# Performance work log

Hardware: AMD Instinct MI355X
Metric: run time of the kernel (lower is better)

Reference implementation:

```python
import jax, jax.numpy as jnp
import numpy as np

NUM_HEADS = 4

def _pos_encoding(seq_len, d, dtype):
    # standard sinusoidal positional encoding [seq_len, d]
    pos = jnp.arange(seq_len, dtype=jnp.float32)[:, None]
    i = jnp.arange(0, d, 2, dtype=jnp.float32)
    div = jnp.exp(-jnp.log(10000.0) * i / d)
    ang = pos * div
    pe = jnp.zeros((seq_len, d), jnp.float32)
    pe = pe.at[:, 0::2].set(jnp.sin(ang)).at[:, 1::2].set(jnp.cos(ang))
    return pe.astype(dtype)

def _layer_norm(x, g, b, eps=1e-5):
    m = jnp.mean(x, axis=-1, keepdims=True)
    v = jnp.mean(jnp.square(x - m), axis=-1, keepdims=True)
    return (x - m) / jnp.sqrt(v + eps) * g + b

def setup_inputs() -> dict:
    key = jax.random.key(0)
    ks = jax.random.split(key, 10)
    B, S, H, W, N = 8, 512, 768, 8, 4096
    s = 0.02
    token_reps = jax.random.normal(ks[0], (B, S, H), jnp.float32)
    starts = jax.random.randint(ks[1], (B, N), 0, S - W)
    widths = jax.random.randint(ks[2], (B, N), 1, W + 1)
    span_ids = jnp.stack([starts, starts + widths], axis=-1)  # end > start, end <= S
    span_masks = jax.random.randint(ks[3], (B, N), 0, 2)
    return dict(
        token_reps=token_reps,
        dummy_query=jax.random.normal(ks[4], (H,), jnp.float32) * s,
        in_proj_w=jax.random.normal(ks[5], (3 * H, H), jnp.float32) * s,
        in_proj_b=jnp.zeros((3 * H,), jnp.float32),
        out_w=jax.random.normal(ks[6], (H, H), jnp.float32) * s,
        out_b=jnp.zeros((H,), jnp.float32),
        ln_g=jnp.ones((H,), jnp.float32),
        ln_b=jnp.zeros((H,), jnp.float32),
        ffn_w1=jax.random.normal(ks[7], (H, 4 * H), jnp.float32) * s,
        ffn_b1=jnp.zeros((4 * H,), jnp.float32),
        ffn_w2=jax.random.normal(ks[8], (4 * H, H), jnp.float32) * s,
        ffn_b2=jnp.zeros((H,), jnp.float32),
        span_ids=span_ids,
        span_masks=span_masks,
    )

def reference(token_reps, dummy_query, in_proj_w, in_proj_b, out_w, out_b,
              ln_g, ln_b, ffn_w1, ffn_b1, ffn_w2, ffn_b2, span_ids, span_masks):
    B, S, H = token_reps.shape
    N = span_ids.shape[1]
    NH = NUM_HEADS
    DH = H // NH
    # sequence positional encoding (dropout is identity in eval mode)
    x = token_reps + _pos_encoding(S, H, token_reps.dtype)[None]
    Wq, Wk, Wv = jnp.split(in_proj_w, 3, axis=0)
    bq, bk, bv = jnp.split(in_proj_b, 3)
    # single shared dummy query -> per-head query [NH, DH]
    q = (dummy_query @ Wq.T + bq).reshape(NH, DH)
    k = (x @ Wk.T + bk).reshape(B, S, NH, DH)
    v = (x @ Wv.T + bv).reshape(B, S, NH, DH)
    # scores are identical across spans since the query is shared: [B, NH, S]
    scores = jnp.einsum('hd,bshd->bhs', q, k) / jnp.sqrt(jnp.asarray(DH, x.dtype))
    pos = jnp.arange(S)
    # per-span key validity: start <= pos < end, and span not masked out  [B, N, S]
    valid = (pos[None, None, :] >= span_ids[..., 0:1]) & \
            (pos[None, None, :] < span_ids[..., 1:2]) & \
            (span_masks[..., None] != 0)
    logits = jnp.where(valid[:, :, None, :], scores[:, None, :, :], -1e9)  # [B,N,NH,S]
    w = jax.nn.softmax(logits, axis=-1)
    attn = jnp.einsum('bnhs,bshd->bnhd', w, v).reshape(B, N, H)
    attn = attn @ out_w.T + out_b
    h1 = _layer_norm(attn + dummy_query, ln_g, ln_b)
    ffn = jax.nn.relu(h1 @ ffn_w1 + ffn_b1) @ ffn_w2 + ffn_b2
    out = _layer_norm(ffn + h1, ln_g, ln_b)
    # masked spans produce exact zeros, matching the original loop
    return out * (span_masks[..., None] != 0).astype(out.dtype)
```

## Files before the change

### kernel.cpp

```cpp
#include <hip/hip_runtime.h>
#include <hip/hip_bf16.h>

#define Bb 8
#define Ss 512
#define Hh 768
#define NHh 4
#define Nn 4096
#define ROWS (Bb * Nn)
#define SCB 128

typedef _Float16 f16x8 __attribute__((ext_vector_type(8)));
typedef _Float16 f16x4 __attribute__((ext_vector_type(4)));
typedef _Float16 f16x2 __attribute__((ext_vector_type(2)));
typedef float f32x4 __attribute__((ext_vector_type(4)));

#define DEVINL __device__ __forceinline__

DEVINL void gld_lds16(const void* g, void* l) {
  __builtin_amdgcn_global_load_lds(
      (const __attribute__((address_space(1))) void*)g,
      (__attribute__((address_space(3))) void*)l, 16, 0, 0);
}

template <int V>
DEVINL void wait_vmcnt() {
  if constexpr (V == 0) asm volatile("s_waitcnt vmcnt(0)" ::: "memory");
  else if constexpr (V == 3) asm volatile("s_waitcnt vmcnt(3)" ::: "memory");
  else if constexpr (V == 4) asm volatile("s_waitcnt vmcnt(4)" ::: "memory");
  else if constexpr (V == 6) asm volatile("s_waitcnt vmcnt(6)" ::: "memory");
  else if constexpr (V == 8) asm volatile("s_waitcnt vmcnt(8)" ::: "memory");
}

DEVINL float block_sum256(float v, float* red) {
#pragma unroll
  for (int o = 32; o; o >>= 1) v += __shfl_xor(v, o, 64);
  const int wid = threadIdx.x >> 6, lane = threadIdx.x & 63;
  if (lane == 0) red[wid] = v;
  __syncthreads();
  float r = red[0] + red[1] + red[2] + red[3];
  __syncthreads();
  return r;
}

__global__ __launch_bounds__(256) void x_kernel(const float* __restrict__ tok,
                                                _Float16* __restrict__ x) {
  int idx = blockIdx.x * 256 + threadIdx.x;
  int t = idx % 384;
  int bs = idx / 384;
  int s = bs & (Ss - 1);
  float div = expf(-(float)t * 0.02398526138535465f);
  float ang = (float)s * div;
  float sv = sinf(ang), cv = cosf(ang);
  const float2 tv = ((const float2*)tok)[(size_t)bs * 384 + t];
  f16x2 o;
  o[0] = (_Float16)(tv.x + sv);
  o[1] = (_Float16)(tv.y + cv);
  *(f16x2*)&x[(size_t)bs * Hh + 2 * t] = o;
}

__global__ __launch_bounds__(256) void q_kernel(const float* __restrict__ dq,
                                                const float* __restrict__ ipw,
                                                const float* __restrict__ ipb,
                                                float* __restrict__ qout) {
  __shared__ float red[4];
  int o = blockIdx.x;
  const float* wr = ipw + (size_t)o * Hh;
  float s = 0.f;
#pragma unroll
  for (int e = 0; e < 3; e++) {
    int j = threadIdx.x + 256 * e;
    s += dq[j] * wr[j];
  }
  s = block_sum256(s, red);
  if (threadIdx.x == 0) qout[o] = s + ipb[o];
}

__global__ __launch_bounds__(256) void c_kernel(const float* __restrict__ q,
                                                const float* __restrict__ ipw,
                                                const float* __restrict__ ipb,
                                                float* __restrict__ cout,
                                                float* __restrict__ sbias) {
  __shared__ float red[4];
  int bid = blockIdx.x;
  int t = threadIdx.x;
  if (bid < 3072) {
    int h = bid / Hh;
    int j = bid - h * Hh;
    float s = 0.f;
    if (t < 192) s = q[h * 192 + t] * ipw[(size_t)(Hh + h * 192 + t) * Hh + j];
    s = block_sum256(s, red);
    if (t == 0) cout[bid] = s;
  } else {
    int h = bid - 3072;
    float s = 0.f;
    if (t < 192) s = q[h * 192 + t] * ipb[Hh + h * 192 + t];
    s = block_sum256(s, red);
    if (t == 0) sbias[h] = s;
  }
}

__global__ __launch_bounds__(256) void score_kernel(
    const _Float16* __restrict__ x, const float* __restrict__ c,
    const float* __restrict__ sbias, float* __restrict__ scores) {
  int bs = blockIdx.x;
  int wid = threadIdx.x >> 6, lane = threadIdx.x & 63;
  const _Float16* xr = x + (size_t)bs * Hh;
  const float* ch = c + wid * Hh;
  float s = 0.f;
#pragma unroll
  for (int e = 0; e < 12; e++) {
    int j = e * 64 + lane;
    s += (float)xr[j] * ch[j];
  }
#pragma unroll
  for (int o = 32; o; o >>= 1) s += __shfl_xor(s, o, 64);
  if (lane == 0) {
    int b = bs >> 9, pos = bs & (Ss - 1);
    scores[((size_t)(b * NHh + wid)) * Ss + pos] =
        (s + sbias[wid]) * 0.07216878364870322f;
  }
}

__global__ __launch_bounds__(256) void cvt_kernel(const float* __restrict__ in,
                                                  _Float16* __restrict__ out) {
  int i = blockIdx.x * 256 + threadIdx.x;
  float4 f = ((const float4*)in)[i];
  f16x4 o;
  o[0] = (_Float16)f.x;
  o[1] = (_Float16)f.y;
  o[2] = (_Float16)f.z;
  o[3] = (_Float16)f.w;
  ((f16x4*)out)[i] = o;
}

__global__ __launch_bounds__(256) void trcvt_kernel(const float* __restrict__ in,
                                                    _Float16* __restrict__ out,
                                                    int R, int C) {
  __shared__ float tile[32][33];
  int c0 = blockIdx.x * 32, r0 = blockIdx.y * 32;
  int tx = threadIdx.x & 31, ty0 = threadIdx.x >> 5;
#pragma unroll
  for (int ty = ty0; ty < 32; ty += 8)
    tile[ty][tx] = in[(size_t)(r0 + ty) * C + c0 + tx];
  __syncthreads();
#pragma unroll
  for (int ty = ty0; ty < 32; ty += 8)
    out[(size_t)(c0 + ty) * R + r0 + tx] = (_Float16)tile[tx][ty];
}

__global__ __launch_bounds__(256) void scan1_kernel(const int* __restrict__ mask,
                                                    int* __restrict__ bsum) {
  int r = blockIdx.x * 256 + threadIdx.x;
  unsigned long long b = __ballot(mask[r] != 0);
  __shared__ int wsum[4];
  int lane = threadIdx.x & 63, wid = threadIdx.x >> 6;
  if (lane == 0) wsum[wid] = __popcll(b);
  __syncthreads();
  if (threadIdx.x == 0)
    bsum[blockIdx.x] = wsum[0] + wsum[1] + wsum[2] + wsum[3];
}
__global__ __launch_bounds__(64) void scan2_kernel(const int* __restrict__ bsum,
                                                   int* __restrict__ boff,
                                                   int* __restrict__ cnt) {
  if (threadIdx.x == 0) {
    int acc = 0;
    for (int i = 0; i < SCB; i++) {
      boff[i] = acc;
      acc += bsum[i];
    }
    *cnt = acc;
  }
}
__global__ __launch_bounds__(256) void cidx_kernel(const int* __restrict__ mask,
                                                   const int* __restrict__ boff,
                                                   int* __restrict__ cidx) {
  int r = blockIdx.x * 256 + threadIdx.x;
  int m = mask[r] != 0;
  unsigned long long b = __ballot(m);
  __shared__ int wsum[4];
  int lane = threadIdx.x & 63, wid = threadIdx.x >> 6;
  if (lane == 0) wsum[wid] = __popcll(b);
  __syncthreads();
  int pre = 0;
#pragma unroll
  for (int i = 0; i < 3; i++)
    if (i < wid) pre += wsum[i];
  pre += __popcll(b & ((1ULL << lane) - 1));
  if (m) cidx[r] = boff[blockIdx.x] + pre;
}

template <int RELU, int BN>
__global__ __launch_bounds__(256, 2) void gemm_nt(
    const _Float16* __restrict__ A, const _Float16* __restrict__ W,
    const float* __restrict__ bias, _Float16* __restrict__ C, int N, int K,
    int nn, const int* __restrict__ mcount) {
  const int bid = (int)blockIdx.x;
  const int mi = (bid >> 3) / nn;
  const int nt_ = (bid >> 3) - mi * nn;
  const long m0 = (long)(mi * 8 + (bid & 7)) * 128;
  const long n0 = (long)nt_ * BN;
  if (mcount && m0 >= (long)*mcount) return;
  __shared__ __align__(16) _Float16 As[3][128 * 32];
  __shared__ __align__(16) _Float16 Bs[3][BN * 32];
  const int tid = threadIdx.x;
  const int wid = tid >> 6;
  const int lane = tid & 63;
  constexpr int LPS = (BN == 128) ? 4 : 3;

  const int c0 = wid * 64 + lane;
  const int c1 = c0 + 256;
  const int sw0 = ((c0 & 3) ^ ((c0 >> 3) & 3)) * 8;
  const int sw1 = ((c1 & 3) ^ ((c1 >> 3) & 3)) * 8;
  const _Float16* gA0 = A + (m0 + (c0 >> 2)) * K + sw0;
  const _Float16* gA1 = A + (m0 + (c1 >> 2)) * K + sw1;
  const _Float16* gB0 = W + (n0 + (c0 >> 2)) * K + sw0;
  const _Float16* gB1 = W + (n0 + (c1 >> 2)) * K + sw1;

  const int wr = (wid >> 1) * 64;
  const int wc = (wid & 1) * (BN / 2);
  constexpr int NF = BN / 32;
  const int fr = lane & 15;
  const int fkb = lane >> 4;

  f32x4 acc[4][NF];
#pragma unroll
  for (int mi2 = 0; mi2 < 4; mi2++)
#pragma unroll
    for (int ni = 0; ni < NF; ni++) acc[mi2][ni] = (f32x4){0.f, 0.f, 0.f, 0.f};

#define STAGE(buf, k0)                                                  \
  do {                                                                  \
    gld_lds16(gA0 + (k0), &As[buf][wid * 512]);                         \
    gld_lds16(gA1 + (k0), &As[buf][2048 + wid * 512]);                  \
    gld_lds16(gB0 + (k0), &Bs[buf][wid * 512]);                         \
    if constexpr (BN == 128) gld_lds16(gB1 + (k0), &Bs[buf][2048 + wid * 512]); \
  } while (0)

#define COMPUTE(buf)                                                          \
  do {                                                                        \
    f16x8 af[4], bf[NF];                                                      \
    _Pragma("unroll") for (int i = 0; i < 4; i++) {                           \
      int r_ = wr + i * 16 + fr;                                              \
      af[i] = *(const f16x8*)&As[buf][r_ * 32 + ((fkb ^ ((r_ >> 1) & 3)) * 8)]; \
    }                                                                         \
    _Pragma("unroll") for (int i = 0; i < NF; i++) {                          \
      int r_ = wc + i * 16 + fr;                                              \
      bf[i] = *(const f16x8*)&Bs[buf][r_ * 32 + ((fkb ^ ((r_ >> 1) & 3)) * 8)]; \
    }                                                                         \
    __builtin_amdgcn_s_setprio(1);                                            \
    _Pragma("unroll") for (int mi2 = 0; mi2 < 4; mi2++)                       \
        _Pragma("unroll") for (int ni = 0; ni < NF; ni++)                     \
            acc[mi2][ni] = __builtin_amdgcn_mfma_f32_16x16x32_f16(            \
                af[mi2], bf[ni], acc[mi2][ni], 0, 0, 0);                      \
    __builtin_amdgcn_s_setprio(0);                                            \
  } while (0)

#define ITER_RESTAGE(b, knext)              \
  do {                                      \
    wait_vmcnt<2 * LPS>();                  \
    __builtin_amdgcn_s_barrier();           \
    COMPUTE(b);                             \
    __builtin_amdgcn_s_barrier();           \
    STAGE(b, (knext));                      \
  } while (0)

  const int nt = K >> 5;
  STAGE(0, 0);
  STAGE(1, 32);
  STAGE(2, 64);
  int t = 0;
  for (; t <= nt - 6; t += 3) {
    ITER_RESTAGE(0, (t + 3) * 32);
    ITER_RESTAGE(1, (t + 4) * 32);
    ITER_RESTAGE(2, (t + 5) * 32);
  }
  wait_vmcnt<2 * LPS>();
  __builtin_amdgcn_s_barrier();
  COMPUTE(0);
  wait_vmcnt<LPS>();
  __builtin_amdgcn_s_barrier();
  COMPUTE(1);
  wait_vmcnt<0>();
  __builtin_amdgcn_s_barrier();
  COMPUTE(2);
#undef STAGE
#undef COMPUTE
#undef ITER_RESTAGE

  const int crow = (lane >> 4) * 4;
  const int ccol = lane & 15;
  float bv[NF];
#pragma unroll
  for (int ni = 0; ni < NF; ni++)
    bv[ni] = bias ? bias[n0 + wc + ni * 16 + ccol] : 0.f;
#pragma unroll
  for (int mi2 = 0; mi2 < 4; mi2++)
#pragma unroll
    for (int ni = 0; ni < NF; ni++)
#pragma unroll
      for (int i = 0; i < 4; i++) {
        float v = acc[mi2][ni][i] + bv[ni];
        if (RELU) v = fmaxf(v, 0.f);
        C[(m0 + wr + mi2 * 16 + crow + i) * (long)N + (n0 + wc + ni * 16 + ccol)] =
            (_Float16)v;
      }
}

__global__ __launch_bounds__(192) void pool_kernel(
    const _Float16* __restrict__ v, const float* __restrict__ scores,
    const int* __restrict__ span_ids, const int* __restrict__ span_masks,
    _Float16* __restrict__ attn, const int* __restrict__ cidx) {
  int r = blockIdx.x;
  if (span_masks[r] == 0) return;
  int slot = cidx[r];
  int i = threadIdx.x;
  int h = i / 48;
  int d0 = i * 4;
  int b = r >> 12;
  int st = span_ids[2 * r], en = span_ids[2 * r + 1];
  int wdt = en - st;
  const float* sc = scores + ((size_t)(b * NHh + h)) * Ss + st;
  float w[8];
  float mx = -1e30f;
#pragma unroll
  for (int j = 0; j < 8; j++) {
    float t = (j < wdt) ? sc[j] : -1e30f;
    w[j] = t;
    mx = fmaxf(mx, t);
  }
  float sum = 0.f;
#pragma unroll
  for (int j = 0; j < 8; j++) {
    float e = (j < wdt) ? expf(w[j] - mx) : 0.f;
    w[j] = e;
    sum += e;
  }
  float inv = 1.f / sum;
  float a0 = 0.f, a1 = 0.f, a2 = 0.f, a3 = 0.f;
#pragma unroll
  for (int j = 0; j < 8; j++) {
    if (j < wdt) {
      f16x4 vv = *(const f16x4*)(v + ((size_t)(b * Ss + st + j)) * Hh + d0);
      float wj = w[j] * inv;
      a0 += wj * (float)vv[0];
      a1 += wj * (float)vv[1];
      a2 += wj * (float)vv[2];
      a3 += wj * (float)vv[3];
    }
  }
  f16x4 o;
  o[0] = (_Float16)a0;
  o[1] = (_Float16)a1;
  o[2] = (_Float16)a2;
  o[3] = (_Float16)a3;
  *(f16x4*)&attn[(size_t)slot * Hh + d0] = o;
}

__global__ __launch_bounds__(256) void ln0_kernel(
    _Float16* __restrict__ X, const float* __restrict__ AddV,
    const float* __restrict__ g, const float* __restrict__ bta,
    const int* __restrict__ mcount) {
  __shared__ float red[4];
  int r = blockIdx.x;
  if (r >= *mcount) return;
  int t = threadIdx.x;
  float xv[3];
#pragma unroll
  for (int e = 0; e < 3; e++) {
    int d = t + 256 * e;
    xv[e] = (float)X[(size_t)r * Hh + d] + AddV[d];
  }
  float s = xv[0] + xv[1] + xv[2];
  s = block_sum256(s, red);
  float mean = s * (1.f / 768.f);
  float vs = 0.f;
#pragma unroll
  for (int e = 0; e < 3; e++) {
    float d = xv[e] - mean;
    vs += d * d;
  }
  vs = block_sum256(vs, red);
  float inv = rsqrtf(vs * (1.f / 768.f) + 1e-5f);
#pragma unroll
  for (int e = 0; e < 3; e++) {
    int d = t + 256 * e;
    X[(size_t)r * Hh + d] = (_Float16)((xv[e] - mean) * inv * g[d] + bta[d]);
  }
}

__global__ __launch_bounds__(256) void ln1_kernel(
    const _Float16* __restrict__ F2c, const _Float16* __restrict__ h1c,
    const int* __restrict__ cidx, const float* __restrict__ g,
    const float* __restrict__ bta, const int* __restrict__ mask,
    float* __restrict__ out) {
  __shared__ float red[4];
  int r = blockIdx.x;
  int t = threadIdx.x;
  float* orow = out + (size_t)r * Hh;
  if (mask[r] == 0) {
#pragma unroll
    for (int e = 0; e < 3; e++) orow[t + 256 * e] = 0.f;
    return;
  }
  int c = cidx[r];
  float xv[3];
#pragma unroll
  for (int e = 0; e < 3; e++) {
    int d = t + 256 * e;
    xv[e] = (float)F2c[(size_t)c * Hh + d] + (float)h1c[(size_t)c * Hh + d];
  }
  float s = xv[0] + xv[1] + xv[2];
  s = block_sum256(s, red);
  float mean = s * (1.f / 768.f);
  float vs = 0.f;
#pragma unroll
  for (int e = 0; e < 3; e++) {
    float d = xv[e] - mean;
    vs += d * d;
  }
  vs = block_sum256(vs, red);
  float inv = rsqrtf(vs * (1.f / 768.f) + 1e-5f);
#pragma unroll
  for (int e = 0; e < 3; e++) {
    int d = t + 256 * e;
    orow[d] = (xv[e] - mean) * inv * g[d] + bta[d];
  }
}

extern "C" void kernel_launch(void* const* d_in, const int* in_sizes, int n_in,
                              void* d_out, int out_size, void* d_ws,
                              size_t ws_size, hipStream_t stream) {
  (void)out_size;
  if (n_in != 14) return;
  if (in_sizes[0] != 3145728 || in_sizes[2] != 1769472 ||
      in_sizes[3] != 2304 || in_sizes[4] != 589824 ||
      in_sizes[8] != 2359296 || in_sizes[9] != 3072 ||
      in_sizes[12] != 65536 || in_sizes[13] != 32768)
    return;

  const float* tok   = (const float*)d_in[0];
  const float* dq    = (const float*)d_in[1];
  const float* ipw   = (const float*)d_in[2];
  const float* ipb   = (const float*)d_in[3];
  const float* outw  = (const float*)d_in[4];
  const float* outb  = (const float*)d_in[5];
  const float* lng   = (const float*)d_in[6];
  const float* lnb   = (const float*)d_in[7];
  const float* w1    = (const float*)d_in[8];
  const float* b1    = (const float*)d_in[9];
  const float* w2    = (const float*)d_in[10];
  const float* b2    = (const float*)d_in[11];
  const int* spid    = (const int*)d_in[12];
  const int* spmask  = (const int*)d_in[13];

  char* ws = (char*)d_ws;
  size_t off = 0;
  auto alloc = [&](size_t bytes) {
    size_t r = off;
    off = (off + bytes + 255) & ~(size_t)255;
    return r;
  };
  _Float16* X16  = (_Float16*)(ws + alloc((size_t)Bb * Ss * Hh * 2));
  float* SC      = (float*)(ws + alloc((size_t)Bb * NHh * Ss * 4));
  float* Q       = (float*)(ws + alloc(768 * 4));
  float* Cc      = (float*)(ws + alloc(3072 * 4));
  float* SB      = (float*)(ws + alloc(4 * 4));
  _Float16* WV16 = (_Float16*)(ws + alloc((size_t)768 * 768 * 2));
  _Float16* OW16 = (_Float16*)(ws + alloc((size_t)768 * 768 * 2));
  _Float16* WT1  = (_Float16*)(ws + alloc((size_t)3072 * 768 * 2));
  _Float16* WT2  = (_Float16*)(ws + alloc((size_t)768 * 3072 * 2));
  _Float16* ATTN = (_Float16*)(ws + alloc((size_t)ROWS * Hh * 2));
  _Float16* PROJ = (_Float16*)(ws + alloc((size_t)ROWS * Hh * 2));
  _Float16* F1   = (_Float16*)(ws + alloc((size_t)ROWS * 3072 * 2));
  if (ws_size < off) return;
  _Float16* F2 = ATTN;

  int* CIDX = (int*)X16;
  int* BSUM = (int*)X16 + ROWS;
  int* BOFF = (int*)X16 + ROWS + SCB;
  int* CNT  = (int*)X16 + ROWS + 2 * SCB;

  _Float16* V16 = (_Float16*)d_out;

  cvt_kernel<<<576, 256, 0, stream>>>(ipw + (size_t)1536 * 768, WV16);
  cvt_kernel<<<576, 256, 0, stream>>>(outw, OW16);
  trcvt_kernel<<<dim3(96, 24), 256, 0, stream>>>(w1, WT1, 768, 3072);
  trcvt_kernel<<<dim3(24, 96), 256, 0, stream>>>(w2, WT2, 3072, 768);

  x_kernel<<<(Bb * Ss * 384) / 256, 256, 0, stream>>>(tok, X16);
  q_kernel<<<768, 256, 0, stream>>>(dq, ipw, ipb, Q);
  c_kernel<<<3076, 256, 0, stream>>>(Q, ipw, ipb, Cc, SB);
  score_kernel<<<Bb * Ss, 256, 0, stream>>>(X16, Cc, SB, SC);
  gemm_nt<0, 64><<<384, 256, 0, stream>>>(X16, WV16, ipb + 1536, V16,
                                          768, 768, 12, nullptr);
  scan1_kernel<<<SCB, 256, 0, stream>>>(spmask, BSUM);
  scan2_kernel<<<1, 64, 0, stream>>>(BSUM, BOFF, CNT);
  cidx_kernel<<<SCB, 256, 0, stream>>>(spmask, BOFF, CIDX);
  pool_kernel<<<ROWS, 192, 0, stream>>>(V16, SC, spid, spmask, ATTN, CIDX);
  gemm_nt<0, 128><<<1536, 256, 0, stream>>>(ATTN, OW16, outb, PROJ,
                                            768, 768, 6, CNT);
  ln0_kernel<<<ROWS, 256, 0, stream>>>(PROJ, dq, lng, lnb, CNT);
  gemm_nt<1, 128><<<6144, 256, 0, stream>>>(PROJ, WT1, b1, F1,
                                            3072, 768, 24, CNT);
  gemm_nt<0, 128><<<1536, 256, 0, stream>>>(F1, WT2, b2, F2,
                                            768, 3072, 6, CNT);
  ln1_kernel<<<ROWS, 256, 0, stream>>>(F2, PROJ, CIDX, lng, lnb, spmask,
                                       (float*)d_out);
}
```

Baseline: 413.5 us.

## Add 256x128-tile 8-wave GEMM with triple-buffered LDS for span MLP

```diff
diff --git a/kernel.cpp b/kernel.cpp
--- a/kernel.cpp
+++ b/kernel.cpp
@@ -306,6 +306,121 @@
       }
 }
 
+template <int RELU>
+__global__ __launch_bounds__(512, 4) void gemm8_nt(
+    const _Float16* __restrict__ A, const _Float16* __restrict__ W,
+    const float* __restrict__ bias, _Float16* __restrict__ C, int N, int K,
+    int nn, const int* __restrict__ mcount) {
+  const int bid = (int)blockIdx.x;
+  const int mi = (bid >> 3) / nn;
+  const int nt_ = (bid >> 3) - mi * nn;
+  const long m0 = (long)(mi * 8 + (bid & 7)) * 256;
+  const long n0 = (long)nt_ * 128;
+  if (mcount && m0 >= (long)*mcount) return;
+  __shared__ __align__(16) _Float16 As[3][256 * 32];
+  __shared__ __align__(16) _Float16 Bs[3][128 * 32];
+  const int tid = threadIdx.x;
+  const int w = tid >> 6;
+  const int lane = tid & 63;
+  constexpr int LPS = 3;
+
+  const int rA0 = w * 16 + (lane >> 2);
+  const int rA1 = rA0 + 128;
+  const int cb = lane & 3;
+  const int swA0 = (cb ^ ((rA0 >> 1) & 3)) * 8;
+  const int swA1 = (cb ^ ((rA1 >> 1) & 3)) * 8;
+  const _Float16* gA0 = A + (m0 + rA0) * K + swA0;
+  const _Float16* gA1 = A + (m0 + rA1) * K + swA1;
+  const _Float16* gB0 = W + (n0 + rA0) * K + swA0;
+
+  const int wr = (w >> 1) * 64;
+  const int wc = (w & 1) * 64;
+  const int fr = lane & 15;
+  const int fkb = lane >> 4;
+
+  f32x4 acc[4][4];
+#pragma unroll
+  for (int mi2 = 0; mi2 < 4; mi2++)
+#pragma unroll
+    for (int ni = 0; ni < 4; ni++) acc[mi2][ni] = (f32x4){0.f, 0.f, 0.f, 0.f};
+
+#define STAGE(buf, k0)                                   \
+  do {                                                   \
+    gld_lds16(gA0 + (k0), &As[buf][w * 512]);            \
+    gld_lds16(gA1 + (k0), &As[buf][(w + 8) * 512]);      \
+    gld_lds16(gB0 + (k0), &Bs[buf][w * 512]);            \
+  } while (0)
+
+#define COMPUTE(buf)                                                          \
+  do {                                                                        \
+    f16x8 af[4], bf[4];                                                       \
+    _Pragma("unroll") for (int i = 0; i < 4; i++) {                           \
+      int r_ = wr + i * 16 + fr;                                              \
+      af[i] = *(const f16x8*)&As[buf][r_ * 32 + ((fkb ^ ((r_ >> 1) & 3)) * 8)]; \
+    }                                                                         \
+    _Pragma("unroll") for (int i = 0; i < 4; i++) {                           \
+      int r_ = wc + i * 16 + fr;                                              \
+      bf[i] = *(const f16x8*)&Bs[buf][r_ * 32 + ((fkb ^ ((r_ >> 1) & 3)) * 8)]; \
+    }                                                                         \
+    __builtin_amdgcn_s_setprio(1);                                            \
+    _Pragma("unroll") for (int mi2 = 0; mi2 < 4; mi2++)                       \
+        _Pragma("unroll") for (int ni = 0; ni < 4; ni++)                      \
+            acc[mi2][ni] = __builtin_amdgcn_mfma_f32_16x16x32_f16(            \
+                af[mi2], bf[ni], acc[mi2][ni], 0, 0, 0);                      \
+    __builtin_amdgcn_s_setprio(0);                                            \
+  } while (0)
+
+#define ITER_RESTAGE(b, knext)              \
+  do {                                      \
+    wait_vmcnt<2 * LPS>();                  \
+    __builtin_amdgcn_s_barrier();           \
+    COMPUTE(b);                             \
+    __builtin_amdgcn_s_barrier();           \
+    STAGE(b, (knext));                      \
+  } while (0)
+
+  const int nt = K >> 5;
+  STAGE(0, 0);
+  STAGE(1, 32);
+  STAGE(2, 64);
+  int t = 0;
+  for (; t <= nt - 6; t += 3) {
+    ITER_RESTAGE(0, (t + 3) * 32);
+    ITER_RESTAGE(1, (t + 4) * 32);
+    ITER_RESTAGE(2, (t + 5) * 32);
+  }
+  wait_vmcnt<2 * LPS>();
+  __builtin_amdgcn_s_barrier();
+  COMPUTE(0);
+  wait_vmcnt<LPS>();
+  __builtin_amdgcn_s_barrier();
+  COMPUTE(1);
+  wait_vmcnt<0>();
+  __builtin_amdgcn_s_barrier();
+  COMPUTE(2);
+#undef STAGE
+#undef COMPUTE
+#undef ITER_RESTAGE
+
+  const int crow = (lane >> 4) * 4;
+  const int ccol = lane & 15;
+  float bv[4];
+#pragma unroll
+  for (int ni = 0; ni < 4; ni++)
+    bv[ni] = bias ? bias[n0 + wc + ni * 16 + ccol] : 0.f;
+#pragma unroll
+  for (int mi2 = 0; mi2 < 4; mi2++)
+#pragma unroll
+    for (int ni = 0; ni < 4; ni++)
+#pragma unroll
+      for (int i = 0; i < 4; i++) {
+        float v = acc[mi2][ni][i] + bv[ni];
+        if (RELU) v = fmaxf(v, 0.f);
+        C[(m0 + wr + mi2 * 16 + crow + i) * (long)N + (n0 + wc + ni * 16 + ccol)] =
+            (_Float16)v;
+      }
+}
+
 __global__ __launch_bounds__(192) void pool_kernel(
     const _Float16* __restrict__ v, const float* __restrict__ scores,
     const int* __restrict__ span_ids, const int* __restrict__ span_masks,
@@ -497,13 +612,13 @@
   scan2_kernel<<<1, 64, 0, stream>>>(BSUM, BOFF, CNT);
   cidx_kernel<<<SCB, 256, 0, stream>>>(spmask, BOFF, CIDX);
   pool_kernel<<<ROWS, 192, 0, stream>>>(V16, SC, spid, spmask, ATTN, CIDX);
-  gemm_nt<0, 128><<<1536, 256, 0, stream>>>(ATTN, OW16, outb, PROJ,
-                                            768, 768, 6, CNT);
+  gemm8_nt<0><<<768, 512, 0, stream>>>(ATTN, OW16, outb, PROJ,
+                                       768, 768, 6, CNT);
   ln0_kernel<<<ROWS, 256, 0, stream>>>(PROJ, dq, lng, lnb, CNT);
-  gemm_nt<1, 128><<<6144, 256, 0, stream>>>(PROJ, WT1, b1, F1,
-                                            3072, 768, 24, CNT);
-  gemm_nt<0, 128><<<1536, 256, 0, stream>>>(F1, WT2, b2, F2,
-                                            768, 3072, 6, CNT);
+  gemm8_nt<1><<<3072, 512, 0, stream>>>(PROJ, WT1, b1, F1,
+                                        3072, 768, 24, CNT);
+  gemm8_nt<0><<<768, 512, 0, stream>>>(F1, WT2, b2, F2,
+                                       768, 3072, 6, CNT);
   ln1_kernel<<<ROWS, 256, 0, stream>>>(F2, PROJ, CIDX, lng, lnb, spmask,
                                        (float*)d_out);
 }
```

After: 365.6 us. 1.13x faster.
